# Kernel tuning notes

Measured on AMD Instinct MI355X. Metric: run time of the kernel, lower is better.

## Reference

```python
import math
import jax, jax.numpy as jnp
import numpy as np

B, H, S, D = 2, 16, 2048, 128

def setup_inputs() -> dict:
    key = jax.random.key(0)
    kq, kk, kv, km = jax.random.split(key, 4)
    q = jax.random.normal(kq, (B, H, S, D), dtype=jnp.float32)
    k = jax.random.normal(kk, (B, H, S, D), dtype=jnp.float32)
    v = jax.random.normal(kv, (B, H, S, D), dtype=jnp.float32)
    mask = jax.random.randint(km, (B, 1, S, S), 0, 2, dtype=jnp.int32)
    return {"q": q, "k": k, "v": v, "mask": mask}

def reference(q, k, v, mask):
    d_tensor = k.shape[-1]
    # score = q @ k^T / sqrt(d)
    score = jnp.einsum("bhqd,bhkd->bhqk", q, k) / jnp.sqrt(jnp.float32(d_tensor))
    # faithful to torch: masked positions are set to 1e-09 (not -inf) before softmax
    score = jnp.where(mask == 0, jnp.float32(1e-09), score)
    score = jax.nn.softmax(score, axis=-1)
    out = jnp.einsum("bhqk,bhkd->bhqd", score, v)
    return (out, score)
```

## Files before the change

kernel.cpp:

```cpp
#include <hip/hip_runtime.h>


#define S_LEN 2048
#define DH 128
#define NT 32
#define SCALE 0.088388347648318447f

typedef short short8_t __attribute__((ext_vector_type(8)));
typedef float f32x4_t __attribute__((ext_vector_type(4)));
typedef unsigned short u16x4_t __attribute__((ext_vector_type(4)));
typedef unsigned int u32x4_t __attribute__((ext_vector_type(4)));

__device__ __forceinline__ unsigned short f2bf(float x) {
  union { float f; unsigned u; } c; c.f = x;
  return (unsigned short)((c.u + 0x7FFFu + ((c.u >> 16) & 1u)) >> 16);
}
__device__ __forceinline__ float bf2f(unsigned short b) {
  union { float f; unsigned u; } c; c.u = ((unsigned)b) << 16;
  return c.f;
}
__device__ __forceinline__ void gll16(const void* g, void* l) {
  __builtin_amdgcn_global_load_lds(
      (const __attribute__((address_space(1))) unsigned int*)g,
      (__attribute__((address_space(3))) unsigned int*)l, 16, 0, 0);
}
__device__ __forceinline__ unsigned pk2(unsigned short a, unsigned short b) {
  return (unsigned)a | ((unsigned)b << 16);
}


__global__ void pack_mask_k(const int* __restrict__ M, unsigned long long* __restrict__ bm) {
  int g = (blockIdx.x * 256 + threadIdx.x) >> 6;
  int lane = threadIdx.x & 63;
#pragma unroll
  for (int i = 0; i < 16; ++i) {
    int w = g * 16 + i;
    int v = M[(size_t)w * 64 + lane];
    unsigned long long bits = __ballot(v != 0);
    if (lane == 0) bm[w] = bits;
  }
}

__global__ void conv_k_k(const float* __restrict__ K, unsigned short* __restrict__ kws) {
  int c = blockIdx.x * 256 + threadIdx.x;
  int tile = c >> 10;
  int p = (c & 1023) * 16;
  int r = p >> 8, X = p & 255;
  int d0 = (X ^ ((r & 7) << 4)) >> 1;
  int bh = tile >> 5, k = (tile & 31) * 64 + r;
  const float* src = K + ((size_t)bh * S_LEN + k) * DH + d0;
  f32x4_t a = *(const f32x4_t*)src;
  f32x4_t b = *(const f32x4_t*)(src + 4);
  u32x4_t o = { pk2(f2bf(a[0]), f2bf(a[1])), pk2(f2bf(a[2]), f2bf(a[3])),
                pk2(f2bf(b[0]), f2bf(b[1])), pk2(f2bf(b[2]), f2bf(b[3])) };
  *(u32x4_t*)((char*)kws + (size_t)tile * 16384 + p) = o;
}

__global__ void conv_v_k(const float* __restrict__ V, unsigned short* __restrict__ vws) {
  __shared__ unsigned short vt[64 * 132];
  int tile = blockIdx.x, bh = tile >> 5, kt = tile & 31;
  int tid = threadIdx.x;
  const float* src = V + ((size_t)bh * S_LEN + kt * 64) * DH;
#pragma unroll
  for (int pass = 0; pass < 8; ++pass) {
    int idx = pass * 256 + tid;
    int row = idx >> 5, d0 = (idx & 31) * 4;
    f32x4_t a = *(const f32x4_t*)(src + (size_t)row * DH + d0);
    u16x4_t w = { f2bf(a[0]), f2bf(a[1]), f2bf(a[2]), f2bf(a[3]) };
    *(u16x4_t*)&vt[row * 132 + d0] = w;
  }
  __syncthreads();
#pragma unroll
  for (int c4 = 0; c4 < 4; ++c4) {
    int chunk = c4 * 256 + tid;
    int p = chunk * 16;
    int d = p >> 7, X = p & 127;
    int kv0 = (X ^ ((d & 7) << 4)) >> 1;
    unsigned short e[8];
#pragma unroll
    for (int i = 0; i < 8; ++i) e[i] = vt[(kv0 + i) * 132 + d];
    u32x4_t o = { pk2(e[0], e[1]), pk2(e[2], e[3]), pk2(e[4], e[5]), pk2(e[6], e[7]) };
    *(u32x4_t*)((char*)vws + (size_t)tile * 16384 + p) = o;
  }
}


__global__ __launch_bounds__(512, 4)
void sdpa_fused(const float* __restrict__ Q,
                const unsigned short* __restrict__ kws,
                const unsigned short* __restrict__ vws,
                const unsigned long long* __restrict__ bm,
                float* __restrict__ Out, float* __restrict__ Sc) {
  extern __shared__ char smem[];
  char* kbb = smem;
  char* vbb = smem + 32768;
  unsigned short* pbB = (unsigned short*)(smem + 65536);
  float* lpart = (float*)(smem + 65536 + 9216);
  float* rinv  = lpart + 128;

  const int tid = threadIdx.x;
  const int lane = tid & 63, wid = tid >> 6;
  const int qh = wid >> 2, kq = wid & 3;
  const int lg = lane >> 4, ln = lane & 15;

  const int wg = blockIdx.x;
  const int j = wg >> 3;
  const int bh = (wg & 7) * 4 + (j >> 6);
  const int qt = j & 63;
  const int b = bh >> 4;
  const int q0 = qt * 32;

  short8_t qf[4];
  {
    const float* qrow = Q + ((size_t)bh * S_LEN + q0 + qh * 16 + ln) * DH;
#pragma unroll
    for (int kk = 0; kk < 4; ++kk) {
      f32x4_t a = *(const f32x4_t*)(qrow + kk * 32 + lg * 8);
      f32x4_t c = *(const f32x4_t*)(qrow + kk * 32 + lg * 8 + 4);
      short8_t f;
#pragma unroll
      for (int jj = 0; jj < 4; ++jj) { f[jj] = (short)f2bf(a[jj]); f[4 + jj] = (short)f2bf(c[jj]); }
      qf[kk] = f;
    }
  }

  const char* ktiles = (const char*)kws + (size_t)bh * NT * 16384;
  const char* vtiles = (const char*)vws + (size_t)bh * NT * 16384;
  const int stoff = wid * 1024 + lane * 16;
  const int ldoff = wid * 1024;

  const unsigned long long* bmr = bm + ((size_t)b * S_LEN + q0 + qh * 16 + lg * 4) * NT;
  const int krow = kq * 16 + ln;
  const int arow = qh * 16 + ln;
  const int bitp = kq * 16 + ln;
  const int pbase = (qh * 16 + lg * 4) * 72 + kq * 16 + ln;

  float psum[4] = {0.f, 0.f, 0.f, 0.f};

  gll16(ktiles + stoff,        kbb + ldoff);
  gll16(ktiles + stoff + 8192, kbb + ldoff + 8192);
  __syncthreads();

#pragma unroll 4
  for (int kt = 0; kt < NT; ++kt) {
    const int cur = kt & 1, nxt = cur ^ 1;
    if (kt < NT - 1) {
      const char* gk = ktiles + (size_t)(kt + 1) * 16384 + stoff;
      gll16(gk,        kbb + nxt * 16384 + ldoff);
      gll16(gk + 8192, kbb + nxt * 16384 + ldoff + 8192);
    }
    unsigned long long mw0 = bmr[kt],          mw1 = bmr[NT + kt];
    unsigned long long mw2 = bmr[2 * NT + kt], mw3 = bmr[3 * NT + kt];

    const char* kbc = kbb + cur * 16384;
    f32x4_t acc = {0.f, 0.f, 0.f, 0.f};
#pragma unroll
    for (int kk = 0; kk < 4; ++kk) {
      short8_t bfr = *(const short8_t*)(kbc + krow * 256 + ((kk * 64 + lg * 16) ^ ((krow & 7) << 4)));
      acc = __builtin_amdgcn_mfma_f32_16x16x32_bf16(qf[kk], bfr, acc, 0, 0, 0);
    }
    psum[0] += ((mw0 >> bitp) & 1) ? __expf(acc[0] * SCALE) : 1.0f;
    psum[1] += ((mw1 >> bitp) & 1) ? __expf(acc[1] * SCALE) : 1.0f;
    psum[2] += ((mw2 >> bitp) & 1) ? __expf(acc[2] * SCALE) : 1.0f;
    psum[3] += ((mw3 >> bitp) & 1) ? __expf(acc[3] * SCALE) : 1.0f;
    __syncthreads();
  }

#pragma unroll
  for (int off = 1; off < 16; off <<= 1) {
#pragma unroll
    for (int jj = 0; jj < 4; ++jj) psum[jj] += __shfl_xor(psum[jj], off, 64);
  }
  if (ln == 0) {
#pragma unroll
    for (int jj = 0; jj < 4; ++jj) lpart[kq * 32 + qh * 16 + lg * 4 + jj] = psum[jj];
  }
  __syncthreads();
  if (tid < 32)
    rinv[tid] = 1.0f / (lpart[tid] + lpart[32 + tid] + lpart[64 + tid] + lpart[96 + tid]);
  __syncthreads();

  const int sr = tid >> 4, sc4 = (tid & 15) * 4;
  const float ri_s = rinv[sr];
  float* scp = Sc + ((size_t)bh * S_LEN + q0 + sr) * S_LEN + sc4;

  gll16(ktiles + stoff,        kbb + ldoff);
  gll16(ktiles + stoff + 8192, kbb + ldoff + 8192);
  gll16(vtiles + stoff,        vbb + ldoff);
  gll16(vtiles + stoff + 8192, vbb + ldoff + 8192);
  __syncthreads();

  f32x4_t oacc0 = {0.f, 0.f, 0.f, 0.f}, oacc1 = {0.f, 0.f, 0.f, 0.f};

#pragma unroll 4
  for (int kt = 0; kt < NT; ++kt) {
    const int cur = kt & 1, nxt = cur ^ 1;
    if (kt < NT - 1) {
      const char* gk = ktiles + (size_t)(kt + 1) * 16384 + stoff;
      const char* gv = vtiles + (size_t)(kt + 1) * 16384 + stoff;
      gll16(gk,        kbb + nxt * 16384 + ldoff);
      gll16(gk + 8192, kbb + nxt * 16384 + ldoff + 8192);
      gll16(gv,        vbb + nxt * 16384 + ldoff);
      gll16(gv + 8192, vbb + nxt * 16384 + ldoff + 8192);
    }
    unsigned long long mw0 = bmr[kt],          mw1 = bmr[NT + kt];
    unsigned long long mw2 = bmr[2 * NT + kt], mw3 = bmr[3 * NT + kt];

    const char* kbc = kbb + cur * 16384;
    f32x4_t acc = {0.f, 0.f, 0.f, 0.f};
#pragma unroll
    for (int kk = 0; kk < 4; ++kk) {
      short8_t bfr = *(const short8_t*)(kbc + krow * 256 + ((kk * 64 + lg * 16) ^ ((krow & 7) << 4)));
      acc = __builtin_amdgcn_mfma_f32_16x16x32_bf16(qf[kk], bfr, acc, 0, 0, 0);
    }
    float p0 = ((mw0 >> bitp) & 1) ? __expf(acc[0] * SCALE) : 1.0f;
    float p1 = ((mw1 >> bitp) & 1) ? __expf(acc[1] * SCALE) : 1.0f;
    float p2 = ((mw2 >> bitp) & 1) ? __expf(acc[2] * SCALE) : 1.0f;
    float p3 = ((mw3 >> bitp) & 1) ? __expf(acc[3] * SCALE) : 1.0f;
    unsigned short* pbc = pbB + cur * 2304;
    pbc[pbase]       = f2bf(p0);
    pbc[pbase + 72]  = f2bf(p1);
    pbc[pbase + 144] = f2bf(p2);
    pbc[pbase + 216] = f2bf(p3);
    asm volatile("s_waitcnt lgkmcnt(0)\n\ts_barrier" ::: "memory");
    {
      u16x4_t w = *(const u16x4_t*)&pbc[sr * 72 + sc4];
      f32x4_t o = { bf2f(w[0]) * ri_s, bf2f(w[1]) * ri_s, bf2f(w[2]) * ri_s, bf2f(w[3]) * ri_s };
      __builtin_nontemporal_store(o, (f32x4_t*)(scp + kt * 64));
    }
    const char* vbc = vbb + cur * 16384;
    short8_t af0 = *(const short8_t*)((const char*)pbc + arow * 144 + lg * 16);
    short8_t af1 = *(const short8_t*)((const char*)pbc + arow * 144 + 64 + lg * 16);
    {
      const int vr0 = kq * 32 + ln;
      short8_t bv0 = *(const short8_t*)(vbc + vr0 * 128 + ((lg * 16) ^ ((vr0 & 7) << 4)));
      short8_t bv1 = *(const short8_t*)(vbc + vr0 * 128 + ((64 + lg * 16) ^ ((vr0 & 7) << 4)));
      oacc0 = __builtin_amdgcn_mfma_f32_16x16x32_bf16(af0, bv0, oacc0, 0, 0, 0);
      oacc0 = __builtin_amdgcn_mfma_f32_16x16x32_bf16(af1, bv1, oacc0, 0, 0, 0);
    }
    {
      const int vr1 = kq * 32 + 16 + ln;
      short8_t bv0 = *(const short8_t*)(vbc + vr1 * 128 + ((lg * 16) ^ ((vr1 & 7) << 4)));
      short8_t bv1 = *(const short8_t*)(vbc + vr1 * 128 + ((64 + lg * 16) ^ ((vr1 & 7) << 4)));
      oacc1 = __builtin_amdgcn_mfma_f32_16x16x32_bf16(af0, bv0, oacc1, 0, 0, 0);
      oacc1 = __builtin_amdgcn_mfma_f32_16x16x32_bf16(af1, bv1, oacc1, 0, 0, 0);
    }
    __syncthreads();
  }

#pragma unroll
  for (int jj = 0; jj < 4; ++jj) {
    int row = qh * 16 + lg * 4 + jj;
    float ri = rinv[row];
    size_t o = ((size_t)bh * S_LEN + q0 + row) * DH + kq * 32 + ln;
    __builtin_nontemporal_store(oacc0[jj] * ri, &Out[o]);
    __builtin_nontemporal_store(oacc1[jj] * ri, &Out[o + 16]);
  }
}


#define PT_STRIDE 2056
#define KLDS_STRIDE 136
#define VT_STRIDE 72

__global__ __launch_bounds__(512, 1)
void sdpa_kernel_v1(const float* __restrict__ Q, const float* __restrict__ K,
                    const float* __restrict__ V, const int* __restrict__ M,
                    float* __restrict__ Out, float* __restrict__ Sc) {
  extern __shared__ char smem[];
  unsigned short* pt  = (unsigned short*)smem;
  unsigned short* kvb = (unsigned short*)(smem + 131584);
  float* lpart = (float*)(smem + 131584 + 18432);
  float* rinv  = lpart + 128;

  const int tid  = threadIdx.x;
  const int lane = tid & 63;
  const int wid  = tid >> 6;
  const int qh = wid >> 2, kq = wid & 3;
  const int lg = lane >> 4, ln = lane & 15;

  const int bid = blockIdx.x;
  const int qt = bid & 63, bh = bid >> 6, b = bh >> 4;
  const int q0 = qt * 32;

  const float* Qb = Q + ((size_t)bh * S_LEN + q0) * DH;
  const float* Kb = K + (size_t)bh * S_LEN * DH;
  const float* Vb = V + (size_t)bh * S_LEN * DH;
  const int*   Mb = M + ((size_t)b * S_LEN + q0) * (size_t)S_LEN;

  short8_t qf[4];
  {
    const float* qrow = Qb + (qh * 16 + ln) * DH;
#pragma unroll
    for (int kk = 0; kk < 4; ++kk) {
      f32x4_t a = *(const f32x4_t*)(qrow + kk * 32 + lg * 8);
      f32x4_t c = *(const f32x4_t*)(qrow + kk * 32 + lg * 8 + 4);
      short8_t f;
#pragma unroll
      for (int jj = 0; jj < 4; ++jj) { f[jj] = (short)f2bf(a[jj]); f[4 + jj] = (short)f2bf(c[jj]); }
      qf[kk] = f;
    }
  }

  float psum[4] = {0.f, 0.f, 0.f, 0.f};

  for (int kt = 0; kt < 32; ++kt) {
    const int k0 = kt * 64;
    __syncthreads();
#pragma unroll
    for (int p = 0; p < 4; ++p) {
      int idx = (p << 11) | (tid << 2);
      int r = idx >> 7, d0 = idx & 127;
      f32x4_t val = *(const f32x4_t*)(Kb + (size_t)(k0 + r) * DH + d0);
      u16x4_t w = { f2bf(val[0]), f2bf(val[1]), f2bf(val[2]), f2bf(val[3]) };
      *(u16x4_t*)&kvb[r * KLDS_STRIDE + d0] = w;
    }
    __syncthreads();

    const int kcol = k0 + kq * 16 + ln;
    int mv[4];
#pragma unroll
    for (int jj = 0; jj < 4; ++jj)
      mv[jj] = Mb[(size_t)(qh * 16 + lg * 4 + jj) * S_LEN + kcol];

    f32x4_t acc = {0.f, 0.f, 0.f, 0.f};
#pragma unroll
    for (int kk = 0; kk < 4; ++kk) {
      short8_t bf = *(short8_t*)&kvb[(kq * 16 + ln) * KLDS_STRIDE + kk * 32 + lg * 8];
      acc = __builtin_amdgcn_mfma_f32_16x16x32_bf16(qf[kk], bf, acc, 0, 0, 0);
    }
#pragma unroll
    for (int jj = 0; jj < 4; ++jj) {
      float p = mv[jj] ? __expf(acc[jj] * SCALE) : 1.0f;
      psum[jj] += p;
      pt[(qh * 16 + lg * 4 + jj) * PT_STRIDE + kcol] = f2bf(p);
    }
  }

#pragma unroll
  for (int off = 1; off < 16; off <<= 1) {
#pragma unroll
    for (int jj = 0; jj < 4; ++jj) psum[jj] += __shfl_xor(psum[jj], off, 64);
  }
  if (ln == 0) {
#pragma unroll
    for (int jj = 0; jj < 4; ++jj) lpart[kq * 32 + qh * 16 + lg * 4 + jj] = psum[jj];
  }
  __syncthreads();
  if (tid < 32)
    rinv[tid] = 1.0f / (lpart[tid] + lpart[32 + tid] + lpart[64 + tid] + lpart[96 + tid]);
  __syncthreads();

  {
    float* srow = Sc + ((size_t)bh * S_LEN + q0) * (size_t)S_LEN;
#pragma unroll 4
    for (int r = 0; r < 32; ++r) {
      float ri = rinv[r];
      u16x4_t w = *(u16x4_t*)&pt[r * PT_STRIDE + tid * 4];
      f32x4_t o = { bf2f(w[0]) * ri, bf2f(w[1]) * ri, bf2f(w[2]) * ri, bf2f(w[3]) * ri };
      *(f32x4_t*)(srow + (size_t)r * S_LEN + tid * 4) = o;
    }
  }

  const int dq = kq;
  f32x4_t oacc0 = {0.f,0.f,0.f,0.f}, oacc1 = {0.f,0.f,0.f,0.f};
  const int dcol = tid & 127, qq = tid >> 7;
  for (int vt = 0; vt < 32; ++vt) {
    const int k0 = vt * 64;
    __syncthreads();
#pragma unroll
    for (int p = 0; p < 4; ++p) {
      int krb = p * 16 + qq * 4;
      const float* vp = Vb + (size_t)(k0 + krb) * DH + dcol;
      float v0 = vp[0], v1 = vp[DH], v2 = vp[2 * DH], v3 = vp[3 * DH];
      u16x4_t w = { f2bf(v0), f2bf(v1), f2bf(v2), f2bf(v3) };
      *(u16x4_t*)&kvb[dcol * VT_STRIDE + krb] = w;
    }
    __syncthreads();
#pragma unroll
    for (int ks = 0; ks < 2; ++ks) {
      short8_t af = *(short8_t*)&pt[(qh * 16 + ln) * PT_STRIDE + k0 + ks * 32 + lg * 8];
#pragma unroll
      for (int nb = 0; nb < 2; ++nb) {
        short8_t bf = *(short8_t*)&kvb[(dq * 32 + nb * 16 + ln) * VT_STRIDE + ks * 32 + lg * 8];
        if (nb == 0) oacc0 = __builtin_amdgcn_mfma_f32_16x16x32_bf16(af, bf, oacc0, 0, 0, 0);
        else         oacc1 = __builtin_amdgcn_mfma_f32_16x16x32_bf16(af, bf, oacc1, 0, 0, 0);
      }
    }
  }
#pragma unroll
  for (int jj = 0; jj < 4; ++jj) {
    int row = qh * 16 + lg * 4 + jj;
    float ri = rinv[row];
    size_t o = ((size_t)bh * S_LEN + q0 + row) * DH + dq * 32 + ln;
    Out[o]      = oacc0[jj] * ri;
    Out[o + 16] = oacc1[jj] * ri;
  }
}


extern "C" void kernel_launch(void* const* d_in, const int* in_sizes, int n_in,
                              void* d_out, int out_size, void* d_ws, size_t ws_size,
                              hipStream_t stream) {
  const float* q = (const float*)d_in[0];
  const float* k = (const float*)d_in[1];
  const float* v = (const float*)d_in[2];
  const int*   m = (const int*)d_in[3];
  float* out = (float*)d_out;
  float* sc  = out + (size_t)2 * 16 * S_LEN * DH;

  const size_t BM_BYTES = 1u << 20;
  const size_t KW_BYTES = (size_t)32 * 32 * 16384;
  const size_t NEED = BM_BYTES + 2 * KW_BYTES;

  if (ws_size >= NEED) {
    unsigned long long* bm = (unsigned long long*)d_ws;
    unsigned short* kws = (unsigned short*)((char*)d_ws + BM_BYTES);
    unsigned short* vws = (unsigned short*)((char*)d_ws + BM_BYTES + KW_BYTES);

    pack_mask_k<<<dim3(2048), dim3(256), 0, stream>>>(m, bm);
    conv_k_k<<<dim3(4096), dim3(256), 0, stream>>>(k, kws);
    conv_v_k<<<dim3(1024), dim3(256), 0, stream>>>(v, vws);

    const int smem = 65536 + 9216 + 512 + 128;
    hipFuncSetAttribute((const void*)sdpa_fused,
                        hipFuncAttributeMaxDynamicSharedMemorySize, smem);
    sdpa_fused<<<dim3(2048), dim3(512), smem, stream>>>(q, kws, vws, bm, out, sc);
  } else {
    const int smem = 131584 + 18432 + 512 + 128;
    hipFuncSetAttribute((const void*)sdpa_kernel_v1,
                        hipFuncAttributeMaxDynamicSharedMemorySize, smem);
    sdpa_kernel_v1<<<dim3(2048), dim3(512), smem, stream>>>(q, k, v, m, out, sc);
  }
}
```

Baseline: 319.4 us.

## Deepen K prefetch to four stages and use counted vmcnt waits with mask prefetch

The first pass (row-sum) now uses a 4-deep ring of K tiles in LDS, keeping three tiles in flight, in place of double buffering. Full __syncthreads are replaced with explicit vmcnt-counted waits plus barriers, so loads issued for later tiles do not have to finish before each iteration ends. Mask words are loaded one iteration ahead in both passes, and sched_barriers pin the instruction order. The hand-tuned vmcnt counts depend on exact load ordering and risk races or stalls if the compiler emits a different number of memory ops, and full unrolling grows code size.

After: 307.4 us. -3.7%, faster.

```diff
diff --git a/kernel.cpp b/kernel.cpp
--- a/kernel.cpp
+++ b/kernel.cpp
@@ -92,8 +92,7 @@
                 const unsigned long long* __restrict__ bm,
                 float* __restrict__ Out, float* __restrict__ Sc) {
   extern __shared__ char smem[];
-  char* kbb = smem;
-  char* vbb = smem + 32768;
+  char* kst = smem;
   unsigned short* pbB = (unsigned short*)(smem + 65536);
   float* lpart = (float*)(smem + 65536 + 9216);
   float* rinv  = lpart + 128;
@@ -137,33 +136,52 @@
 
   float psum[4] = {0.f, 0.f, 0.f, 0.f};
 
-  gll16(ktiles + stoff,        kbb + ldoff);
-  gll16(ktiles + stoff + 8192, kbb + ldoff + 8192);
-  __syncthreads();
-
-#pragma unroll 4
+  gll16(ktiles + stoff,                 kst + ldoff);
+  gll16(ktiles + stoff + 8192,          kst + ldoff + 8192);
+  gll16(ktiles + 16384 + stoff,         kst + 16384 + ldoff);
+  gll16(ktiles + 16384 + stoff + 8192,  kst + 16384 + ldoff + 8192);
+  gll16(ktiles + 32768 + stoff,         kst + 32768 + ldoff);
+  gll16(ktiles + 32768 + stoff + 8192,  kst + 32768 + ldoff + 8192);
+  __builtin_amdgcn_sched_barrier(0);
+  unsigned long long ma0 = bmr[0], ma1 = bmr[NT], ma2 = bmr[2 * NT], ma3 = bmr[3 * NT];
+  asm volatile("s_waitcnt vmcnt(8) lgkmcnt(0)\n\ts_barrier" ::: "memory");
+  __builtin_amdgcn_sched_barrier(0);
+
+#pragma unroll
   for (int kt = 0; kt < NT; ++kt) {
-    const int cur = kt & 1, nxt = cur ^ 1;
+    if (kt < NT - 3) {
+      const char* gk = ktiles + (size_t)(kt + 3) * 16384 + stoff;
+      char* dst = kst + ((kt + 3) & 3) * 16384 + ldoff;
+      gll16(gk, dst);
+      gll16(gk + 8192, dst + 8192);
+    }
+    __builtin_amdgcn_sched_barrier(0);
+    unsigned long long c0 = ma0, c1 = ma1, c2 = ma2, c3 = ma3;
     if (kt < NT - 1) {
-      const char* gk = ktiles + (size_t)(kt + 1) * 16384 + stoff;
-      gll16(gk,        kbb + nxt * 16384 + ldoff);
-      gll16(gk + 8192, kbb + nxt * 16384 + ldoff + 8192);
-    }
-    unsigned long long mw0 = bmr[kt],          mw1 = bmr[NT + kt];
-    unsigned long long mw2 = bmr[2 * NT + kt], mw3 = bmr[3 * NT + kt];
-
-    const char* kbc = kbb + cur * 16384;
+      ma0 = bmr[kt + 1]; ma1 = bmr[NT + kt + 1];
+      ma2 = bmr[2 * NT + kt + 1]; ma3 = bmr[3 * NT + kt + 1];
+    }
+    const char* kbc = kst + (kt & 3) * 16384;
     f32x4_t acc = {0.f, 0.f, 0.f, 0.f};
 #pragma unroll
     for (int kk = 0; kk < 4; ++kk) {
       short8_t bfr = *(const short8_t*)(kbc + krow * 256 + ((kk * 64 + lg * 16) ^ ((krow & 7) << 4)));
       acc = __builtin_amdgcn_mfma_f32_16x16x32_bf16(qf[kk], bfr, acc, 0, 0, 0);
     }
-    psum[0] += ((mw0 >> bitp) & 1) ? __expf(acc[0] * SCALE) : 1.0f;
-    psum[1] += ((mw1 >> bitp) & 1) ? __expf(acc[1] * SCALE) : 1.0f;
-    psum[2] += ((mw2 >> bitp) & 1) ? __expf(acc[2] * SCALE) : 1.0f;
-    psum[3] += ((mw3 >> bitp) & 1) ? __expf(acc[3] * SCALE) : 1.0f;
-    __syncthreads();
+    psum[0] += ((c0 >> bitp) & 1) ? __expf(acc[0] * SCALE) : 1.0f;
+    psum[1] += ((c1 >> bitp) & 1) ? __expf(acc[1] * SCALE) : 1.0f;
+    psum[2] += ((c2 >> bitp) & 1) ? __expf(acc[2] * SCALE) : 1.0f;
+    psum[3] += ((c3 >> bitp) & 1) ? __expf(acc[3] * SCALE) : 1.0f;
+    if (kt == 0) {
+      asm volatile("s_waitcnt vmcnt(12) lgkmcnt(0)\n\ts_barrier" ::: "memory");
+    } else if (kt <= 28) {
+      asm volatile("s_waitcnt vmcnt(16) lgkmcnt(0)\n\ts_barrier" ::: "memory");
+    } else if (kt == 29) {
+      asm volatile("s_waitcnt vmcnt(14) lgkmcnt(0)\n\ts_barrier" ::: "memory");
+    } else if (kt == 30) {
+      asm volatile("s_waitcnt vmcnt(12) lgkmcnt(0)\n\ts_barrier" ::: "memory");
+    }
+    __builtin_amdgcn_sched_barrier(0);
   }
 
 #pragma unroll
@@ -180,6 +198,8 @@
     rinv[tid] = 1.0f / (lpart[tid] + lpart[32 + tid] + lpart[64 + tid] + lpart[96 + tid]);
   __syncthreads();
 
+  char* kbb = kst;
+  char* vbb = kst + 32768;
   const int sr = tid >> 4, sc4 = (tid & 15) * 4;
   const float ri_s = rinv[sr];
   float* scp = Sc + ((size_t)bh * S_LEN + q0 + sr) * S_LEN + sc4;
@@ -188,11 +208,14 @@
   gll16(ktiles + stoff + 8192, kbb + ldoff + 8192);
   gll16(vtiles + stoff,        vbb + ldoff);
   gll16(vtiles + stoff + 8192, vbb + ldoff + 8192);
-  __syncthreads();
+  __builtin_amdgcn_sched_barrier(0);
+  ma0 = bmr[0]; ma1 = bmr[NT]; ma2 = bmr[2 * NT]; ma3 = bmr[3 * NT];
+  asm volatile("s_waitcnt vmcnt(4) lgkmcnt(0)\n\ts_barrier" ::: "memory");
+  __builtin_amdgcn_sched_barrier(0);
 
   f32x4_t oacc0 = {0.f, 0.f, 0.f, 0.f}, oacc1 = {0.f, 0.f, 0.f, 0.f};
 
-#pragma unroll 4
+#pragma unroll 2
   for (int kt = 0; kt < NT; ++kt) {
     const int cur = kt & 1, nxt = cur ^ 1;
     if (kt < NT - 1) {
@@ -203,9 +226,12 @@
       gll16(gv,        vbb + nxt * 16384 + ldoff);
       gll16(gv + 8192, vbb + nxt * 16384 + ldoff + 8192);
     }
-    unsigned long long mw0 = bmr[kt],          mw1 = bmr[NT + kt];
-    unsigned long long mw2 = bmr[2 * NT + kt], mw3 = bmr[3 * NT + kt];
-
+    __builtin_amdgcn_sched_barrier(0);
+    unsigned long long c0 = ma0, c1 = ma1, c2 = ma2, c3 = ma3;
+    if (kt < NT - 1) {
+      ma0 = bmr[kt + 1]; ma1 = bmr[NT + kt + 1];
+      ma2 = bmr[2 * NT + kt + 1]; ma3 = bmr[3 * NT + kt + 1];
+    }
     const char* kbc = kbb + cur * 16384;
     f32x4_t acc = {0.f, 0.f, 0.f, 0.f};
 #pragma unroll
@@ -213,16 +239,17 @@
       short8_t bfr = *(const short8_t*)(kbc + krow * 256 + ((kk * 64 + lg * 16) ^ ((krow & 7) << 4)));
       acc = __builtin_amdgcn_mfma_f32_16x16x32_bf16(qf[kk], bfr, acc, 0, 0, 0);
     }
-    float p0 = ((mw0 >> bitp) & 1) ? __expf(acc[0] * SCALE) : 1.0f;
-    float p1 = ((mw1 >> bitp) & 1) ? __expf(acc[1] * SCALE) : 1.0f;
-    float p2 = ((mw2 >> bitp) & 1) ? __expf(acc[2] * SCALE) : 1.0f;
-    float p3 = ((mw3 >> bitp) & 1) ? __expf(acc[3] * SCALE) : 1.0f;
+    float p0 = ((c0 >> bitp) & 1) ? __expf(acc[0] * SCALE) : 1.0f;
+    float p1 = ((c1 >> bitp) & 1) ? __expf(acc[1] * SCALE) : 1.0f;
+    float p2 = ((c2 >> bitp) & 1) ? __expf(acc[2] * SCALE) : 1.0f;
+    float p3 = ((c3 >> bitp) & 1) ? __expf(acc[3] * SCALE) : 1.0f;
     unsigned short* pbc = pbB + cur * 2304;
     pbc[pbase]       = f2bf(p0);
     pbc[pbase + 72]  = f2bf(p1);
     pbc[pbase + 144] = f2bf(p2);
     pbc[pbase + 216] = f2bf(p3);
     asm volatile("s_waitcnt lgkmcnt(0)\n\ts_barrier" ::: "memory");
+    __builtin_amdgcn_sched_barrier(0);
     {
       u16x4_t w = *(const u16x4_t*)&pbc[sr * 72 + sc4];
       f32x4_t o = { bf2f(w[0]) * ri_s, bf2f(w[1]) * ri_s, bf2f(w[2]) * ri_s, bf2f(w[3]) * ri_s };
@@ -245,7 +272,8 @@
       oacc1 = __builtin_amdgcn_mfma_f32_16x16x32_bf16(af0, bv0, oacc1, 0, 0, 0);
       oacc1 = __builtin_amdgcn_mfma_f32_16x16x32_bf16(af1, bv1, oacc1, 0, 0, 0);
     }
-    __syncthreads();
+    asm volatile("s_waitcnt vmcnt(5) lgkmcnt(0)\n\ts_barrier" ::: "memory");
+    __builtin_amdgcn_sched_barrier(0);
   }
 
 #pragma unroll
```
